# Optimization experiments

Hardware: AMD Instinct MI355X
Metric: run time of the kernel (lower is better)

The kernel has to match this reference:

```python
import jax, jax.numpy as jnp
import numpy as np

WIN_SEC, HOP_SEC = 1.0, 0.5


def _plan(lens, T):
    """Host-side replica of the per-sample window planning in seg_from_frames.

    lengths_sec is consumed via .item() in the original torch code, i.e. it is a
    host-side constant that only determines integer slice indices. We compute
    start/end frame indices and the validity mask with numpy, then do a single
    vectorized cumsum-based segment mean on device.
    """
    dur = np.maximum(np.asarray(lens, dtype=np.float64), 0.001)
    fps = T / dur
    win = np.maximum(1, np.round(fps * WIN_SEC).astype(np.int64))   # [B]
    hop = np.maximum(1, np.round(fps * HOP_SEC).astype(np.int64))   # [B]
    n = np.where(T >= win, (T - win) // hop + 1, 0)
    fallback = n == 0            # torch fallback: single mean over all T frames
    n_eff = np.maximum(n, 1)
    maxS = int(n_eff.max())
    s = np.arange(maxS)[None, :] * hop[:, None]                     # [B, maxS]
    start = np.where(fallback[:, None], 0, s)
    end = np.where(fallback[:, None], T, s + win[:, None])
    start = np.minimum(start, T)   # clamp padded slots (masked out anyway)
    end = np.minimum(end, T)
    mask = np.arange(maxS)[None, :] < n_eff[:, None]                # [B, maxS]
    return start, end, mask


def setup_inputs() -> dict:
    key = jax.random.key(0)
    k1, k2 = jax.random.split(key)
    B, T, D = 32, 1500, 768
    H = jax.random.normal(k1, (B, T, D), dtype=jnp.float32)
    lengths_sec = 5.0 + 25.0 * jax.random.uniform(k2, (B,), dtype=jnp.float32)
    return {"H": H, "lengths_sec": lengths_sec}


def reference(H, lengths_sec):
    B, T, D = H.shape
    start, end, mask = _plan(np.asarray(lengths_sec), T)
    # inclusive prefix sums with leading zero: C[b, t] = sum(H[b, :t])  [B, T+1, D]
    C = jnp.concatenate([jnp.zeros((B, 1, D), H.dtype), jnp.cumsum(H, axis=1)], axis=1)
    b = jnp.arange(B)[:, None]                                       # [B, 1]
    seg_sum = C[b, jnp.asarray(end)] - C[b, jnp.asarray(start)]       # [B, maxS, D]
    count = jnp.asarray(np.maximum(end - start, 1), H.dtype)[:, :, None]
    m = jnp.asarray(mask)
    S_pad = (seg_sum / count) * m[:, :, None].astype(H.dtype)         # zero-pad ragged tail
    return S_pad, m
```

## Files before the change

### kernel.cpp

```cpp
#include <hip/hip_runtime.h>


#define BDIM 192

__global__ __launch_bounds__(BDIM)
void seg_mean_kernel(const float4* __restrict__ H4,
                     const float*  __restrict__ lens,
                     float4* __restrict__ S4,
                     float*  __restrict__ M,
                     int T, int maxS) {
    const int D4  = BDIM;
    const int b   = blockIdx.x / maxS;
    const int s   = blockIdx.x % maxS;
    const int tid = threadIdx.x;

    double dur = (double)lens[b];
    if (dur < 0.001) dur = 0.001;
    double fps = (double)T / dur;
    long long win = (long long)rint(fps * 1.0);
    if (win < 1) win = 1;
    long long hop = (long long)rint(fps * 0.5);
    if (hop < 1) hop = 1;
    long long n = ((long long)T >= win) ? (((long long)T - win) / hop + 1) : 0;
    const bool fallback = (n == 0);
    const long long n_eff = fallback ? 1 : n;

    if (tid == 0) {
        M[(size_t)b * maxS + s] = (s < n_eff) ? 1.0f : 0.0f;
    }

    float4* out = S4 + ((size_t)b * maxS + s) * D4;

    if (s >= n_eff) {
        out[tid] = make_float4(0.f, 0.f, 0.f, 0.f);
        return;
    }

    long long start = fallback ? 0 : (long long)s * hop;
    long long end   = fallback ? (long long)T : start + win;
    if (start > T) start = T;
    if (end   > T) end   = T;
    long long cnt = end - start;
    if (cnt < 1) cnt = 1;

    const float4* base = H4 + (size_t)b * T * D4 + tid;

    float ax = 0.f, ay = 0.f, az = 0.f, aw = 0.f;
    float bx = 0.f, by = 0.f, bz = 0.f, bw = 0.f;

    long long t = start;
    for (; t + 8 <= end; t += 8) {
        float4 v0 = base[(t + 0) * D4];
        float4 v1 = base[(t + 1) * D4];
        float4 v2 = base[(t + 2) * D4];
        float4 v3 = base[(t + 3) * D4];
        float4 v4 = base[(t + 4) * D4];
        float4 v5 = base[(t + 5) * D4];
        float4 v6 = base[(t + 6) * D4];
        float4 v7 = base[(t + 7) * D4];
        ax += v0.x + v1.x + v2.x + v3.x;
        ay += v0.y + v1.y + v2.y + v3.y;
        az += v0.z + v1.z + v2.z + v3.z;
        aw += v0.w + v1.w + v2.w + v3.w;
        bx += v4.x + v5.x + v6.x + v7.x;
        by += v4.y + v5.y + v6.y + v7.y;
        bz += v4.z + v5.z + v6.z + v7.z;
        bw += v4.w + v5.w + v6.w + v7.w;
    }
    for (; t < end; ++t) {
        float4 v = base[t * D4];
        ax += v.x; ay += v.y; az += v.z; aw += v.w;
    }

    const float c = (float)cnt;
    out[tid] = make_float4((ax + bx) / c, (ay + by) / c,
                           (az + bz) / c, (aw + bw) / c);
}

extern "C" void kernel_launch(void* const* d_in, const int* in_sizes, int n_in,
                              void* d_out, int out_size, void* d_ws, size_t ws_size,
                              hipStream_t stream) {
    const float* H    = (const float*)d_in[0];
    const float* lens = (const float*)d_in[1];

    const int B = in_sizes[1];
    const int D = 768;
    const int T = in_sizes[0] / (B * D);
    const int maxS = out_size / (B * (D + 1));

    float* S = (float*)d_out;
    float* M = S + (size_t)B * maxS * D;

    dim3 grid(B * maxS);
    seg_mean_kernel<<<grid, BDIM, 0, stream>>>(
        (const float4*)H, lens, (float4*)S, M, T, maxS);
}
```

Measured before the change: 233.5 us.

## Split segment means into hop-chunk partial sums plus per-window combine

Adds a first kernel that sums H over non-overlapping hop-sized chunks into a workspace. A second kernel forms each window mean by adding two adjacent chunk sums and correcting for rounding with a few direct frame reads. This avoids re-reading H for overlapping windows, roughly halving HBM traffic. In exchange it adds a second launch, workspace traffic, and relies on the ncmax sizing covering all chunks.

```diff
diff --git a/kernel.cpp b/kernel.cpp
--- a/kernel.cpp
+++ b/kernel.cpp
@@ -1,55 +1,43 @@
 #include <hip/hip_runtime.h>
 
 
-#define BDIM 192
+#define D4 192
 
-__global__ __launch_bounds__(BDIM)
-void seg_mean_kernel(const float4* __restrict__ H4,
-                     const float*  __restrict__ lens,
-                     float4* __restrict__ S4,
-                     float*  __restrict__ M,
-                     int T, int maxS) {
-    const int D4  = BDIM;
-    const int b   = blockIdx.x / maxS;
-    const int s   = blockIdx.x % maxS;
+__device__ __forceinline__ void plan(double len, int T,
+                                     long long& win, long long& hop) {
+    double dur = (len < 0.001) ? 0.001 : len;
+    double fps = (double)T / dur;
+    win = (long long)rint(fps * 1.0);
+    if (win < 1) win = 1;
+    hop = (long long)rint(fps * 0.5);
+    if (hop < 1) hop = 1;
+}
+
+__global__ __launch_bounds__(D4)
+void chunk_sum_kernel(const float4* __restrict__ H4,
+                      const float*  __restrict__ lens,
+                      float4* __restrict__ P,
+                      int T, int ncmax) {
+    const int b   = blockIdx.x / ncmax;
+    const int c   = blockIdx.x % ncmax;
     const int tid = threadIdx.x;
 
-    double dur = (double)lens[b];
-    if (dur < 0.001) dur = 0.001;
-    double fps = (double)T / dur;
-    long long win = (long long)rint(fps * 1.0);
-    if (win < 1) win = 1;
-    long long hop = (long long)rint(fps * 0.5);
-    if (hop < 1) hop = 1;
-    long long n = ((long long)T >= win) ? (((long long)T - win) / hop + 1) : 0;
-    const bool fallback = (n == 0);
-    const long long n_eff = fallback ? 1 : n;
+    long long win, hop;
+    plan((double)lens[b], T, win, hop);
+    const long long nc = ((long long)T + hop - 1) / hop;
+    if (c >= nc) return;
 
-    if (tid == 0) {
-        M[(size_t)b * maxS + s] = (s < n_eff) ? 1.0f : 0.0f;
-    }
-
-    float4* out = S4 + ((size_t)b * maxS + s) * D4;
-
-    if (s >= n_eff) {
-        out[tid] = make_float4(0.f, 0.f, 0.f, 0.f);
-        return;
-    }
-
-    long long start = fallback ? 0 : (long long)s * hop;
-    long long end   = fallback ? (long long)T : start + win;
-    if (start > T) start = T;
-    if (end   > T) end   = T;
-    long long cnt = end - start;
-    if (cnt < 1) cnt = 1;
+    const long long r0 = (long long)c * hop;
+    long long r1 = r0 + hop;
+    if (r1 > T) r1 = T;
 
     const float4* base = H4 + (size_t)b * T * D4 + tid;
 
     float ax = 0.f, ay = 0.f, az = 0.f, aw = 0.f;
     float bx = 0.f, by = 0.f, bz = 0.f, bw = 0.f;
 
-    long long t = start;
-    for (; t + 8 <= end; t += 8) {
+    long long t = r0;
+    for (; t + 8 <= r1; t += 8) {
         float4 v0 = base[(t + 0) * D4];
         float4 v1 = base[(t + 1) * D4];
         float4 v2 = base[(t + 2) * D4];
@@ -67,14 +55,76 @@
         bz += v4.z + v5.z + v6.z + v7.z;
         bw += v4.w + v5.w + v6.w + v7.w;
     }
-    for (; t < end; ++t) {
+    for (; t < r1; ++t) {
         float4 v = base[t * D4];
         ax += v.x; ay += v.y; az += v.z; aw += v.w;
     }
 
+    P[((size_t)b * ncmax + c) * D4 + tid] =
+        make_float4(ax + bx, ay + by, az + bz, aw + bw);
+}
+
+__global__ __launch_bounds__(D4)
+void seg_out_kernel(const float4* __restrict__ H4,
+                    const float*  __restrict__ lens,
+                    const float4* __restrict__ P,
+                    float4* __restrict__ S4,
+                    float*  __restrict__ M,
+                    int T, int maxS, int ncmax) {
+    const int b   = blockIdx.x / maxS;
+    const int s   = blockIdx.x % maxS;
+    const int tid = threadIdx.x;
+
+    long long win, hop;
+    plan((double)lens[b], T, win, hop);
+    const long long n = ((long long)T >= win) ? (((long long)T - win) / hop + 1) : 0;
+    const bool fallback = (n == 0);
+    const long long n_eff = fallback ? 1 : n;
+
+    if (tid == 0) M[(size_t)b * maxS + s] = (s < n_eff) ? 1.0f : 0.0f;
+
+    float4* out = S4 + ((size_t)b * maxS + s) * D4;
+    if (s >= n_eff) { out[tid] = make_float4(0.f, 0.f, 0.f, 0.f); return; }
+
+    const float4* Pb = P + (size_t)b * ncmax * D4;
+    const float4* Hb = H4 + (size_t)b * T * D4 + tid;
+
+    float ax, ay, az, aw;
+    long long cnt;
+
+    if (fallback) {
+        const long long nc = ((long long)T + hop - 1) / hop;
+        ax = ay = az = aw = 0.f;
+        for (long long c = 0; c < nc; ++c) {
+            float4 p = Pb[c * D4 + tid];
+            ax += p.x; ay += p.y; az += p.z; aw += p.w;
+        }
+        cnt = T;
+    } else {
+        const long long start = (long long)s * hop;
+        const long long end   = start + win;
+        float4 p = Pb[(size_t)s * D4 + tid];
+        ax = p.x; ay = p.y; az = p.z; aw = p.w;
+        const long long pos = (s + 1) * hop;
+        if (pos < end) {
+            float4 q = Pb[(size_t)(s + 1) * D4 + tid];
+            ax += q.x; ay += q.y; az += q.z; aw += q.w;
+            long long e1 = (s + 2) * hop;
+            if (e1 > T) e1 = T;
+            for (long long r = end; r < e1; ++r) {
+                float4 v = Hb[r * D4];
+                ax -= v.x; ay -= v.y; az -= v.z; aw -= v.w;
+            }
+            for (long long r = e1; r < end; ++r) {
+                float4 v = Hb[r * D4];
+                ax += v.x; ay += v.y; az += v.z; aw += v.w;
+            }
+        }
+        cnt = win;
+    }
+
     const float c = (float)cnt;
-    out[tid] = make_float4((ax + bx) / c, (ay + by) / c,
-                           (az + bz) / c, (aw + bw) / c);
+    out[tid] = make_float4(ax / c, ay / c, az / c, aw / c);
 }
 
 extern "C" void kernel_launch(void* const* d_in, const int* in_sizes, int n_in,
@@ -88,10 +138,14 @@
     const int T = in_sizes[0] / (B * D);
     const int maxS = out_size / (B * (D + 1));
 
+    const int ncmax = maxS + 3;
+
     float* S = (float*)d_out;
     float* M = S + (size_t)B * maxS * D;
+    float4* P = (float4*)d_ws;
 
-    dim3 grid(B * maxS);
-    seg_mean_kernel<<<grid, BDIM, 0, stream>>>(
-        (const float4*)H, lens, (float4*)S, M, T, maxS);
+    chunk_sum_kernel<<<dim3(B * ncmax), D4, 0, stream>>>(
+        (const float4*)H, lens, P, T, ncmax);
+    seg_out_kernel<<<dim3(B * maxS), D4, 0, stream>>>(
+        (const float4*)H, lens, P, (float4*)S, M, T, maxS, ncmax);
 }
```

New measurement: 221.6 us. 1.05x faster.
